# Kernel tuning notes

Hardware: AMD Instinct MI355X
Metric: run time of the kernel (lower is better)

Reference implementation:

```python
import jax, jax.numpy as jnp
import numpy as np

B, Q, K, H, DQ, DK, DV = 8, 256, 256, 256, 256, 256, 256


def setup_inputs() -> dict:
    key = jax.random.key(0)
    k1, k2, k3, k4, k5, k6, k7 = jax.random.split(key, 7)
    queries = jax.random.normal(k1, (B, Q, DQ), dtype=jnp.float32)
    keys = jax.random.normal(k2, (B, K, DK), dtype=jnp.float32)
    values = jax.random.normal(k3, (B, K, DV), dtype=jnp.float32)
    valid_lens = jax.random.randint(k4, (B,), 1, K + 1)
    # learned params (torch Linear without bias); stored as (in, out)
    s = 1.0 / np.sqrt(H)
    W_q = jax.random.uniform(k5, (DQ, H), minval=-s, maxval=s, dtype=jnp.float32)
    W_k = jax.random.uniform(k6, (DK, H), minval=-s, maxval=s, dtype=jnp.float32)
    w_v = jax.random.uniform(k7, (H,), minval=-s, maxval=s, dtype=jnp.float32)
    return {"queries": queries, "keys": keys, "values": values,
            "valid_lens": valid_lens, "W_q": W_q, "W_k": W_k, "w_v": w_v}


def reference(queries, keys, values, valid_lens, W_q, W_k, w_v):
    q = queries @ W_q                      # (B, Q, H)
    k = keys @ W_k                         # (B, K, H)
    # broadcast add + tanh -> (B, Q, K, H), then linear score -> (B, Q, K)
    features = jnp.tanh(q[:, :, None, :] + k[:, None, :, :])
    scores = jnp.einsum('bqkh,h->bqk', features, w_v)
    mask = jnp.arange(K)[None, None, :] >= valid_lens[:, None, None]  # (B,1,K)
    scores = jnp.where(mask, -1000000.0, scores)
    attn = jax.nn.softmax(scores, axis=-1)  # (B, Q, K)
    return jnp.einsum('bqk,bkd->bqd', attn, values)  # (B, Q, DV)
```

## Files before the change

kernel.cpp:

```cpp
#include <hip/hip_runtime.h>
#include <hip/hip_bf16.h>

#define LOG2E 1.4426950408889634f
#define C2    (2.0f * LOG2E)

static __device__ __forceinline__ float fast_exp2(float x) {
#if __has_builtin(__builtin_amdgcn_exp2f)
  return __builtin_amdgcn_exp2f(x);
#else
  return exp2f(x);
#endif
}
static __device__ __forceinline__ float fast_rcp(float x) {
#if __has_builtin(__builtin_amdgcn_rcpf)
  return __builtin_amdgcn_rcpf(x);
#else
  return 1.0f / x;
#endif
}

__global__ __launch_bounds__(256) void proj_kernel(
    const float* __restrict__ queries, const float* __restrict__ keys,
    const float* __restrict__ W_q,     const float* __restrict__ W_k,
    const int*   __restrict__ vlen,
    float* __restrict__ qs, float* __restrict__ ks_p)
{
  const int bz = blockIdx.z;
  const float* X = bz ? keys : queries;
  const float* W = bz ? W_k  : W_q;
  const int n0 = blockIdx.x * 64;
  const int m0 = blockIdx.y * 32;

  if (bz == 1) {
    const int vl = vlen[m0 >> 8];
    if ((m0 & 255) >= vl) return;
  }

  const int t  = threadIdx.x;
  const int tx = t & 15, ty = t >> 4;

  __shared__ __align__(16) float Xs[32 * 34];
  __shared__ __align__(16) float Ws[32 * 68];

  float4 acc0 = make_float4(0.f, 0.f, 0.f, 0.f);
  float4 acc1 = make_float4(0.f, 0.f, 0.f, 0.f);

  for (int kc = 0; kc < 8; ++kc) {
    {
      int row = t >> 3, seg = t & 7;
      float4 v = *(const float4*)&X[(m0 + row) * 256 + kc * 32 + seg * 4];
      Xs[(seg * 4 + 0) * 34 + row] = v.x;
      Xs[(seg * 4 + 1) * 34 + row] = v.y;
      Xs[(seg * 4 + 2) * 34 + row] = v.z;
      Xs[(seg * 4 + 3) * 34 + row] = v.w;
    }
#pragma unroll
    for (int m = 0; m < 2; ++m) {
      int idx = t + 256 * m;
      int row = idx >> 4, seg = idx & 15;
      *(float4*)&Ws[row * 68 + seg * 4] =
          *(const float4*)&W[(kc * 32 + row) * 256 + n0 + seg * 4];
    }
    __syncthreads();
#pragma unroll
    for (int kk = 0; kk < 32; ++kk) {
      float2 a  = *(const float2*)&Xs[kk * 34 + ty * 2];
      float4 bv = *(const float4*)&Ws[kk * 68 + tx * 4];
      acc0.x = fmaf(a.x, bv.x, acc0.x);
      acc0.y = fmaf(a.x, bv.y, acc0.y);
      acc0.z = fmaf(a.x, bv.z, acc0.z);
      acc0.w = fmaf(a.x, bv.w, acc0.w);
      acc1.x = fmaf(a.y, bv.x, acc1.x);
      acc1.y = fmaf(a.y, bv.y, acc1.y);
      acc1.z = fmaf(a.y, bv.z, acc1.z);
      acc1.w = fmaf(a.y, bv.w, acc1.w);
    }
    __syncthreads();
  }

  float4 o0 = make_float4(fast_exp2(acc0.x * C2), fast_exp2(acc0.y * C2),
                          fast_exp2(acc0.z * C2), fast_exp2(acc0.w * C2));
  float4 o1 = make_float4(fast_exp2(acc1.x * C2), fast_exp2(acc1.y * C2),
                          fast_exp2(acc1.z * C2), fast_exp2(acc1.w * C2));
  if (bz == 0) {
    *(float4*)&qs[(m0 + ty * 2 + 0) * 256 + n0 + tx * 4] = o0;
    *(float4*)&qs[(m0 + ty * 2 + 1) * 256 + n0 + tx * 4] = o1;
  } else {
    const int b  = m0 >> 8;
    const int kl = (m0 & 255) + ty * 2;
    float* base = &ks_p[((size_t)(b * 64 + (n0 >> 2) + tx) * 256 + kl) * 4];
    *(float4*)&base[0] = o0;
    *(float4*)&base[4] = o1;
  }
}

template <int NJ>
__device__ __forceinline__ void score_loop(
    const float* __restrict__ kp,
    const float* __restrict__ qp0, const float* __restrict__ qp1,
    const float* __restrict__ wvp, int h4b, float (&sc)[4][2])
{
#pragma unroll 2
  for (int h4 = h4b; h4 < h4b + 16; ++h4) {
    float4 kv[NJ];
#pragma unroll
    for (int j = 0; j < NJ; ++j)
      kv[j] = *(const float4*)(kp + h4 * 1024 + j * 256);
    float4 qv0 = *(const float4*)(qp0 + h4 * 4);
    float4 qv1 = *(const float4*)(qp1 + h4 * 4);
    float4 wv  = *(const float4*)(wvp + h4 * 4);
#pragma unroll
    for (int j = 0; j < NJ; ++j) {
      sc[j][0] = fmaf(wv.x, fast_rcp(fmaf(qv0.x, kv[j].x, 1.f)), sc[j][0]);
      sc[j][1] = fmaf(wv.x, fast_rcp(fmaf(qv1.x, kv[j].x, 1.f)), sc[j][1]);
      sc[j][0] = fmaf(wv.y, fast_rcp(fmaf(qv0.y, kv[j].y, 1.f)), sc[j][0]);
      sc[j][1] = fmaf(wv.y, fast_rcp(fmaf(qv1.y, kv[j].y, 1.f)), sc[j][1]);
      sc[j][0] = fmaf(wv.z, fast_rcp(fmaf(qv0.z, kv[j].z, 1.f)), sc[j][0]);
      sc[j][1] = fmaf(wv.z, fast_rcp(fmaf(qv1.z, kv[j].z, 1.f)), sc[j][1]);
      sc[j][0] = fmaf(wv.w, fast_rcp(fmaf(qv0.w, kv[j].w, 1.f)), sc[j][0]);
      sc[j][1] = fmaf(wv.w, fast_rcp(fmaf(qv1.w, kv[j].w, 1.f)), sc[j][1]);
    }
  }
}

__global__ __launch_bounds__(256, 4) void attn_kernel(
    const float* __restrict__ qs, const float* __restrict__ ks_p,
    const float* __restrict__ values, const int* __restrict__ vlen,
    const float* __restrict__ w_v, float* __restrict__ out)
{
  const int t    = threadIdx.x;
  const int lane = t & 63;
  const int hq   = t >> 6;
  const int bx   = blockIdx.x;
  const int b    = ((bx & 7) + (bx >> 8)) & 7;
  const int q0   = (bx >> 3) * 2;

  __shared__ __align__(16) float sbuf[2048];
  __shared__ __align__(8)  float p2[512];
  __shared__ float rsum_lds[2];

  const int vl = vlen[b];
  const int nj = (vl + 63) >> 6;

  float s0 = w_v[lane] + w_v[lane + 64] + w_v[lane + 128] + w_v[lane + 192];
#pragma unroll
  for (int off = 32; off; off >>= 1) s0 += __shfl_xor(s0, off);
  const float Wsum = s0;

  const float* qp0 = qs + (size_t)(b * 256 + q0) * 256;
  const float* qp1 = qp0 + 256;
  const float* kp  = ks_p + (size_t)b * 65536 + lane * 4;
  const int h4b = hq * 16;

  float sc[4][2] = {};
  switch (nj) {
    case 1:  score_loop<1>(kp, qp0, qp1, w_v, h4b, sc); break;
    case 2:  score_loop<2>(kp, qp0, qp1, w_v, h4b, sc); break;
    case 3:  score_loop<3>(kp, qp0, qp1, w_v, h4b, sc); break;
    default: score_loop<4>(kp, qp0, qp1, w_v, h4b, sc); break;
  }

#pragma unroll
  for (int j = 0; j < 4; ++j)
    *(float2*)&sbuf[((hq * 4 + j) * 64 + lane) * 2] =
        make_float2(sc[j][0], sc[j][1]);
  __syncthreads();

  if (hq < 2) {
    const int q = hq;
    float scores[4];
    float mx = -3.4e38f;
#pragma unroll 4
    for (int j = 0; j < nj; ++j) {
      float s = sbuf[((0 * 4 + j) * 64 + lane) * 2 + q] +
                sbuf[((1 * 4 + j) * 64 + lane) * 2 + q] +
                sbuf[((2 * 4 + j) * 64 + lane) * 2 + q] +
                sbuf[((3 * 4 + j) * 64 + lane) * 2 + q];
      float v = Wsum - 2.f * s;
      if (j * 64 + lane >= vl) v = -1000000.0f;
      scores[j] = v;
      mx = fmaxf(mx, v);
    }
#pragma unroll
    for (int off = 32; off; off >>= 1) mx = fmaxf(mx, __shfl_xor(mx, off));
    float sum = 0.f;
#pragma unroll 4
    for (int j = 0; j < nj; ++j) {
      float p = fast_exp2((scores[j] - mx) * LOG2E);
      p2[(j * 64 + lane) * 2 + q] = p;
      sum += p;
    }
#pragma unroll
    for (int off = 32; off; off >>= 1) sum += __shfl_xor(sum, off);
    if (lane == 0) rsum_lds[q] = sum;
  }
  __syncthreads();

  float4 a0 = make_float4(0.f, 0.f, 0.f, 0.f);
  float4 a1 = make_float4(0.f, 0.f, 0.f, 0.f);
  const float* Vb = values + (size_t)b * 65536 + lane * 4;
#pragma unroll 2
  for (int k = hq; k < vl; k += 4) {
    float2 pk = *(const float2*)&p2[k * 2];
    float4 v  = *(const float4*)(Vb + (size_t)k * 256);
    a0.x = fmaf(pk.x, v.x, a0.x);
    a0.y = fmaf(pk.x, v.y, a0.y);
    a0.z = fmaf(pk.x, v.z, a0.z);
    a0.w = fmaf(pk.x, v.w, a0.w);
    a1.x = fmaf(pk.y, v.x, a1.x);
    a1.y = fmaf(pk.y, v.y, a1.y);
    a1.z = fmaf(pk.y, v.z, a1.z);
    a1.w = fmaf(pk.y, v.w, a1.w);
  }
  *(float4*)&sbuf[(hq * 2 + 0) * 256 + lane * 4] = a0;
  *(float4*)&sbuf[(hq * 2 + 1) * 256 + lane * 4] = a1;
  __syncthreads();

#pragma unroll
  for (int rep = 0; rep < 2; ++rep) {
    int o = t + rep * 256;
    int q = o >> 8, d = o & 255;
    float s = sbuf[(0 + q) * 256 + d] + sbuf[(2 + q) * 256 + d] +
              sbuf[(4 + q) * 256 + d] + sbuf[(6 + q) * 256 + d];
    out[(b * 256 + q0 + q) * 256 + d] = s * fast_rcp(rsum_lds[q]);
  }
}

extern "C" void kernel_launch(void* const* d_in, const int* in_sizes, int n_in,
                              void* d_out, int out_size, void* d_ws, size_t ws_size,
                              hipStream_t stream) {
  const float* queries = (const float*)d_in[0];
  const float* keys    = (const float*)d_in[1];
  const float* values  = (const float*)d_in[2];
  const int*   vlenp   = (const int*)d_in[3];
  const float* W_q     = (const float*)d_in[4];
  const float* W_k     = (const float*)d_in[5];
  const float* w_v     = (const float*)d_in[6];
  float* out = (float*)d_out;

  float* qs   = (float*)d_ws;
  float* ks_p = qs + 2048 * 256;

  dim3 pgrid(4, 64, 2);
  proj_kernel<<<pgrid, 256, 0, stream>>>(queries, keys, W_q, W_k, vlenp, qs, ks_p);
  attn_kernel<<<1024, 256, 0, stream>>>(qs, ks_p, values, vlenp, w_v, out);
}
```

Baseline: 41.33 us.

## Use bf16 MFMA for query/key projection GEMM with repacked weight tile

Replaces the FP32 FMA tiled projection GEMM with bf16 MFMA 16x16x32 instructions. Weights for a 16-column slice are converted to bf16 and packed into shared memory in MFMA operand layout, and X rows are loaded straight from global memory and converted in registers. The grid is retiled to 16x64 output tiles. This cuts ALU cost in the projection stage, but bf16 rounding of inputs feeds exp/tanh features and may hurt accuracy, and each X row is now reread by 16 column blocks.

```diff
diff --git a/kernel.cpp b/kernel.cpp
--- a/kernel.cpp
+++ b/kernel.cpp
@@ -19,7 +19,16 @@
 #endif
 }
 
-__global__ __launch_bounds__(256) void proj_kernel(
+typedef short bf16x8 __attribute__((ext_vector_type(8)));
+typedef float f32x4  __attribute__((ext_vector_type(4)));
+
+static __device__ __forceinline__ short f2bf(float x) {
+  unsigned u = __float_as_uint(x);
+  u += 0x7fff + ((u >> 16) & 1);
+  return (short)(u >> 16);
+}
+
+__global__ __launch_bounds__(256, 4) void proj_kernel(
     const float* __restrict__ queries, const float* __restrict__ keys,
     const float* __restrict__ W_q,     const float* __restrict__ W_k,
     const int*   __restrict__ vlen,
@@ -28,69 +37,64 @@
   const int bz = blockIdx.z;
   const float* X = bz ? keys : queries;
   const float* W = bz ? W_k  : W_q;
-  const int n0 = blockIdx.x * 64;
-  const int m0 = blockIdx.y * 32;
+  const int n0 = blockIdx.x * 16;
+  const int m0 = blockIdx.y * 64;
 
   if (bz == 1) {
     const int vl = vlen[m0 >> 8];
     if ((m0 & 255) >= vl) return;
   }
 
-  const int t  = threadIdx.x;
-  const int tx = t & 15, ty = t >> 4;
-
-  __shared__ __align__(16) float Xs[32 * 34];
-  __shared__ __align__(16) float Ws[32 * 68];
-
-  float4 acc0 = make_float4(0.f, 0.f, 0.f, 0.f);
-  float4 acc1 = make_float4(0.f, 0.f, 0.f, 0.f);
-
+  const int t = threadIdx.x;
+  const int l = t & 63;
+  const int w = t >> 6;
+
+  __shared__ short Wp[8 * 64 * 8];
+
+  {
+    const int krow = t >> 2, nseg = t & 3;
+#pragma unroll
+    for (int p = 0; p < 4; ++p) {
+      const int k = p * 64 + krow;
+      float4 v = *(const float4*)&W[k * 256 + n0 + nseg * 4];
+      const int kc = k >> 5, grp = (k & 31) >> 3, j = k & 7;
+      const int lbase = grp * 16 + nseg * 4;
+      Wp[(kc * 64 + lbase + 0) * 8 + j] = f2bf(v.x);
+      Wp[(kc * 64 + lbase + 1) * 8 + j] = f2bf(v.y);
+      Wp[(kc * 64 + lbase + 2) * 8 + j] = f2bf(v.z);
+      Wp[(kc * 64 + lbase + 3) * 8 + j] = f2bf(v.w);
+    }
+  }
+  __syncthreads();
+
+  const int mb   = m0 + w * 16;
+  const int row  = mb + (l & 15);
+  const int kofs = (l >> 4) * 8;
+
+  f32x4 acc = {0.f, 0.f, 0.f, 0.f};
+#pragma unroll
   for (int kc = 0; kc < 8; ++kc) {
-    {
-      int row = t >> 3, seg = t & 7;
-      float4 v = *(const float4*)&X[(m0 + row) * 256 + kc * 32 + seg * 4];
-      Xs[(seg * 4 + 0) * 34 + row] = v.x;
-      Xs[(seg * 4 + 1) * 34 + row] = v.y;
-      Xs[(seg * 4 + 2) * 34 + row] = v.z;
-      Xs[(seg * 4 + 3) * 34 + row] = v.w;
-    }
-#pragma unroll
-    for (int m = 0; m < 2; ++m) {
-      int idx = t + 256 * m;
-      int row = idx >> 4, seg = idx & 15;
-      *(float4*)&Ws[row * 68 + seg * 4] =
-          *(const float4*)&W[(kc * 32 + row) * 256 + n0 + seg * 4];
-    }
-    __syncthreads();
-#pragma unroll
-    for (int kk = 0; kk < 32; ++kk) {
-      float2 a  = *(const float2*)&Xs[kk * 34 + ty * 2];
-      float4 bv = *(const float4*)&Ws[kk * 68 + tx * 4];
-      acc0.x = fmaf(a.x, bv.x, acc0.x);
-      acc0.y = fmaf(a.x, bv.y, acc0.y);
-      acc0.z = fmaf(a.x, bv.z, acc0.z);
-      acc0.w = fmaf(a.x, bv.w, acc0.w);
-      acc1.x = fmaf(a.y, bv.x, acc1.x);
-      acc1.y = fmaf(a.y, bv.y, acc1.y);
-      acc1.z = fmaf(a.y, bv.z, acc1.z);
-      acc1.w = fmaf(a.y, bv.w, acc1.w);
-    }
-    __syncthreads();
-  }
-
-  float4 o0 = make_float4(fast_exp2(acc0.x * C2), fast_exp2(acc0.y * C2),
-                          fast_exp2(acc0.z * C2), fast_exp2(acc0.w * C2));
-  float4 o1 = make_float4(fast_exp2(acc1.x * C2), fast_exp2(acc1.y * C2),
-                          fast_exp2(acc1.z * C2), fast_exp2(acc1.w * C2));
-  if (bz == 0) {
-    *(float4*)&qs[(m0 + ty * 2 + 0) * 256 + n0 + tx * 4] = o0;
-    *(float4*)&qs[(m0 + ty * 2 + 1) * 256 + n0 + tx * 4] = o1;
-  } else {
-    const int b  = m0 >> 8;
-    const int kl = (m0 & 255) + ty * 2;
-    float* base = &ks_p[((size_t)(b * 64 + (n0 >> 2) + tx) * 256 + kl) * 4];
-    *(float4*)&base[0] = o0;
-    *(float4*)&base[4] = o1;
+    float4 a0 = *(const float4*)&X[(size_t)row * 256 + kc * 32 + kofs];
+    float4 a1 = *(const float4*)&X[(size_t)row * 256 + kc * 32 + kofs + 4];
+    bf16x8 af;
+    af[0] = f2bf(a0.x); af[1] = f2bf(a0.y); af[2] = f2bf(a0.z); af[3] = f2bf(a0.w);
+    af[4] = f2bf(a1.x); af[5] = f2bf(a1.y); af[6] = f2bf(a1.z); af[7] = f2bf(a1.w);
+    bf16x8 bfv = *(bf16x8*)&Wp[(kc * 64 + l) * 8];
+    acc = __builtin_amdgcn_mfma_f32_16x16x32_bf16(af, bfv, acc, 0, 0, 0);
+  }
+
+  const int c = l & 15;
+#pragma unroll
+  for (int j = 0; j < 4; ++j) {
+    const int rj = (l >> 4) * 4 + j;
+    const float o = fast_exp2(acc[j] * C2);
+    if (bz == 0) {
+      qs[(size_t)(mb + rj) * 256 + n0 + c] = o;
+    } else {
+      const int b  = mb >> 8;
+      const int kl = (mb & 255) + rj;
+      ks_p[((size_t)(b * 64 + ((n0 + c) >> 2)) * 256 + kl) * 4 + (c & 3)] = o;
+    }
   }
 }
 
@@ -241,7 +245,7 @@
   float* qs   = (float*)d_ws;
   float* ks_p = qs + 2048 * 256;
 
-  dim3 pgrid(4, 64, 2);
+  dim3 pgrid(16, 32, 2);
   proj_kernel<<<pgrid, 256, 0, stream>>>(queries, keys, W_q, W_k, vlenp, qs, ks_p);
   attn_kernel<<<1024, 256, 0, stream>>>(qs, ks_p, values, vlenp, w_v, out);
 }
```

After: 40.83 us. Within noise of the previous version (-1.2%).
